# Kernel optimization log

Hardware: AMD Instinct MI355X
Metric: run time of the kernel (lower is better)

The kernel has to match this reference:

```python
import jax, jax.numpy as jnp
import numpy as np

E = 1024
H = 16
EPS = 1e-5


def setup_inputs() -> dict:
    key = jax.random.key(0)
    ks = jax.random.split(key, 17)
    B, T = 8, 1024
    s = 0.02
    inp = {
        'x': jax.random.normal(ks[0], (B, T, E), dtype=jnp.float32),
        'Wq': jax.random.normal(ks[1], (E, E), dtype=jnp.float32) * s,
        'bq': jnp.zeros((E,), jnp.float32),
        'Wk': jax.random.normal(ks[2], (E, E), dtype=jnp.float32) * s,
        'bk': jnp.zeros((E,), jnp.float32),
        'Wv': jax.random.normal(ks[3], (E, E), dtype=jnp.float32) * s,
        'bv': jnp.zeros((E,), jnp.float32),
        'Wo': jax.random.normal(ks[4], (E, E), dtype=jnp.float32) * s,
        'bo': jnp.zeros((E,), jnp.float32),
        'W1': jax.random.normal(ks[5], (E, 4 * E), dtype=jnp.float32) * s,
        'b1': jnp.zeros((4 * E,), jnp.float32),
        'W2': jax.random.normal(ks[6], (4 * E, E), dtype=jnp.float32) * s,
        'b2': jnp.zeros((E,), jnp.float32),
        'g1': jnp.ones((E,), jnp.float32),
        'be1': jnp.zeros((E,), jnp.float32),
        'g2': jnp.ones((E,), jnp.float32),
        'be2': jnp.zeros((E,), jnp.float32),
    }
    return inp


def _layernorm(x, g, b):
    mu = jnp.mean(x, axis=-1, keepdims=True)
    var = jnp.mean(jnp.square(x - mu), axis=-1, keepdims=True)
    return (x - mu) * jax.lax.rsqrt(var + EPS) * g + b


def _block(x, Wq, bq, Wk, bk, Wv, bv, Wo, bo, W1, b1, W2, b2, g1, be1, g2, be2):
    B, T, Ee = x.shape
    hd = Ee // H
    q = (x @ Wq + bq).reshape(B, T, H, hd).transpose(0, 2, 1, 3)  # (B,H,T,d)
    k = (x @ Wk + bk).reshape(B, T, H, hd).transpose(0, 2, 1, 3)
    v = (x @ Wv + bv).reshape(B, T, H, hd).transpose(0, 2, 1, 3)
    scores = jnp.einsum('bhqd,bhkd->bhqk', q, k) / jnp.sqrt(jnp.float32(hd))
    causal = jnp.tril(jnp.ones((T, T), bool))
    scores = jnp.where(causal, scores, -jnp.inf)
    w = jax.nn.softmax(scores, axis=-1)
    attn = jnp.einsum('bhqk,bhkd->bhqd', w, v)
    attn = attn.transpose(0, 2, 1, 3).reshape(B, T, Ee)
    attn = attn @ Wo + bo  # dropout is identity (p=0 / eval)
    x = _layernorm(x + attn, g1, be1)
    ff = jax.nn.relu(x @ W1 + b1) @ W2 + b2
    x = _layernorm(x + ff, g2, be2)
    return x


def reference(x, Wq, bq, Wk, bk, Wv, bv, Wo, bo, W1, b1, W2, b2, g1, be1, g2, be2):
    return _block(x, Wq, bq, Wk, bk, Wv, bv, Wo, bo, W1, b1, W2, b2, g1, be1, g2, be2)
```

## Files before the change

### kernel.cpp

```cpp
#include <hip/hip_runtime.h>
#include <math.h>

typedef unsigned short u16;
typedef __attribute__((ext_vector_type(8))) short short8;
typedef __attribute__((ext_vector_type(4))) float floatx4;

__device__ __forceinline__ u16 f2bf(float f) {
    unsigned u = __float_as_uint(f);
    unsigned r = u + 0x7fffu + ((u >> 16) & 1u);
    return (u16)(r >> 16);
}

__device__ __forceinline__ void gload16(const u16* g, u16* l) {
    __builtin_amdgcn_global_load_lds((const __attribute__((address_space(1))) void*)g,
                                     (__attribute__((address_space(3))) void*)l, 16, 0, 0);
}

template<int EPI>
__global__ __launch_bounds__(256) void gemm_mfma(
    const u16* __restrict__ A, const u16* __restrict__ Bt,
    const float* __restrict__ bias, const float* __restrict__ bias2,
    const float* __restrict__ bias3, const float* __restrict__ R,
    void* __restrict__ Cout, void* __restrict__ out2, void* __restrict__ out3,
    int M, int N, int K) {
    __shared__ u16 As[128 * 32];
    __shared__ u16 Bs[128 * 32];
    const int tid = threadIdx.x;
    const int wave = tid >> 6, lane = tid & 63;
    const int lrow = lane & 15, quad = lane >> 4;
    const int m0 = blockIdx.y * 128, n0 = blockIdx.x * 128;
    const int wm = (wave & 1) * 64, wn = (wave >> 1) * 64;

    floatx4 acc[4][4];
#pragma unroll
    for (int i = 0; i < 4; i++)
#pragma unroll
        for (int j = 0; j < 4; j++) acc[i][j] = {0.f, 0.f, 0.f, 0.f};

    const int f0 = wave * 128 + lane;

    for (int k0 = 0; k0 < K; k0 += 32) {
        __syncthreads();
#pragma unroll
        for (int i = 0; i < 2; i++) {
            int f = f0 + i * 64;
            int row = f >> 2, c = f & 3;
            int cg = c ^ ((row >> 1) & 3);
            gload16(A + (size_t)(m0 + row) * K + k0 + cg * 8, As + f * 8);
            gload16(Bt + (size_t)(n0 + row) * K + k0 + cg * 8, Bs + f * 8);
        }
        __syncthreads();
        short8 af[4], bf[4];
#pragma unroll
        for (int mt = 0; mt < 4; mt++) {
            int row = wm + mt * 16 + lrow;
            int ch = quad ^ ((lrow >> 1) & 3);
            af[mt] = *(const short8*)(As + row * 32 + ch * 8);
        }
#pragma unroll
        for (int nt = 0; nt < 4; nt++) {
            int row = wn + nt * 16 + lrow;
            int ch = quad ^ ((lrow >> 1) & 3);
            bf[nt] = *(const short8*)(Bs + row * 32 + ch * 8);
        }
#pragma unroll
        for (int mt = 0; mt < 4; mt++)
#pragma unroll
            for (int nt = 0; nt < 4; nt++)
                acc[mt][nt] = __builtin_amdgcn_mfma_f32_16x16x32_bf16(af[mt], bf[nt], acc[mt][nt], 0, 0, 0);
    }

    const float* bp = bias;
    int sec = 0;
    if (EPI == 4) {
        sec = n0 >> 10;
        bp = sec == 0 ? bias : (sec == 1 ? bias2 : bias3);
    }
    float bv[4];
#pragma unroll
    for (int nt = 0; nt < 4; nt++) {
        int gc = n0 + wn + nt * 16 + lrow;
        bv[nt] = bp[EPI == 4 ? (gc & 1023) : gc];
    }

#pragma unroll
    for (int mt = 0; mt < 4; mt++) {
        int gr0 = m0 + wm + mt * 16 + quad * 4;
#pragma unroll
        for (int nt = 0; nt < 4; nt++) {
            int gc = n0 + wn + nt * 16 + lrow;
            floatx4 a = acc[mt][nt];
            if (EPI == 1) {
                u16* C = (u16*)Cout;
#pragma unroll
                for (int r = 0; r < 4; r++)
                    C[(size_t)(gr0 + r) * N + gc] = f2bf(fmaxf(a[r] + bv[nt], 0.f));
            } else if (EPI == 2) {
                float* C = (float*)Cout;
#pragma unroll
                for (int r = 0; r < 4; r++) {
                    size_t idx = (size_t)(gr0 + r) * N + gc;
                    C[idx] = a[r] + bv[nt] + R[idx];
                }
            } else {
                int nc = gc & 1023;
                if (sec < 2) {
                    u16* C = (u16*)(sec == 0 ? Cout : out2);
#pragma unroll
                    for (int r = 0; r < 4; r++)
                        C[(size_t)(gr0 + r) * 1024 + nc] = f2bf(a[r] + bv[nt]);
                } else {
                    u16* C = (u16*)out3;
                    int bb = gr0 >> 10, t0 = gr0 & 1023;
                    size_t idx = ((size_t)(bb * 1024 + nc)) * 1024 + t0;
                    ushort4 u;
                    u.x = f2bf(a[0] + bv[nt]); u.y = f2bf(a[1] + bv[nt]);
                    u.z = f2bf(a[2] + bv[nt]); u.w = f2bf(a[3] + bv[nt]);
                    *(ushort4*)(C + idx) = u;
                }
            }
        }
    }
}

__global__ __launch_bounds__(256) void attn_mfma(
    const u16* __restrict__ q, const u16* __restrict__ k,
    const u16* __restrict__ vT, u16* __restrict__ o) {
    __shared__ u16 Kb[2][64 * 64];
    __shared__ u16 Vb[2][64 * 64];
    __shared__ u16 Pb[4][2][16 * 72];

    const int tid = threadIdx.x;
    const int wave = tid >> 6, lane = tid & 63;
    const int lrow = lane & 15, quad = lane >> 4;
    const int qb = blockIdx.x, bh = blockIdx.y;
    const int b = bh >> 4, h = bh & 15;
    const size_t tokbase = (size_t)b * 1024;
    const int ktmax = qb * 2 + 1;

#pragma unroll
    for (int i = 0; i < 2; i++) {
        int f = wave * 128 + i * 64 + lane;
        int row = f >> 3, c = f & 7, cg = c ^ (row & 7);
        gload16(q + (tokbase + qb * 128 + row) * 1024 + h * 64 + cg * 8, Kb[1] + f * 8);
        gload16(q + (tokbase + qb * 128 + 64 + row) * 1024 + h * 64 + cg * 8, Vb[1] + f * 8);
        gload16(k + (tokbase + row) * 1024 + h * 64 + cg * 8, Kb[0] + f * 8);
        gload16(vT + (tokbase + h * 64 + row) * 1024 + cg * 8, Vb[0] + f * 8);
    }
    asm volatile("s_waitcnt vmcnt(0)" ::: "memory");
    __syncthreads();
    short8 aQ[2][2];
#pragma unroll
    for (int band = 0; band < 2; band++)
#pragma unroll
        for (int ks = 0; ks < 2; ks++) {
            int row = wave * 16 + lrow;
            int pos = (ks * 4 + quad) ^ (lrow & 7);
            const u16* src = band ? Vb[1] : Kb[1];
            aQ[band][ks] = *(const short8*)(src + row * 64 + pos * 8);
        }
    __syncthreads();

    float lp[2][4];
    floatx4 oa[2][4];
#pragma unroll
    for (int bd = 0; bd < 2; bd++)
#pragma unroll
        for (int i = 0; i < 4; i++) { lp[bd][i] = 0.f; oa[bd][i] = {0.f, 0.f, 0.f, 0.f}; }

    for (int kt = 0; kt <= ktmax; kt++) {
        const int cur = kt & 1;
        if (kt < ktmax) {
            const int nxt = cur ^ 1;
#pragma unroll
            for (int i = 0; i < 2; i++) {
                int f = wave * 128 + i * 64 + lane;
                int row = f >> 3, c = f & 7, cg = c ^ (row & 7);
                gload16(k + (tokbase + (kt + 1) * 64 + row) * 1024 + h * 64 + cg * 8, Kb[nxt] + f * 8);
                gload16(vT + (tokbase + h * 64 + row) * 1024 + (kt + 1) * 64 + cg * 8, Vb[nxt] + f * 8);
            }
        }
#pragma unroll
        for (int band = 0; band < 2; band++) {
            const int btile = qb * 2 + band;
            if (kt > btile) continue;
            floatx4 sacc[4];
#pragma unroll
            for (int nt = 0; nt < 4; nt++) sacc[nt] = {0.f, 0.f, 0.f, 0.f};
#pragma unroll
            for (int nt = 0; nt < 4; nt++)
#pragma unroll
                for (int ks = 0; ks < 2; ks++) {
                    int row = nt * 16 + lrow;
                    int pos = (ks * 4 + quad) ^ (lrow & 7);
                    short8 bK = *(const short8*)(Kb[cur] + row * 64 + pos * 8);
                    sacc[nt] = __builtin_amdgcn_mfma_f32_16x16x32_bf16(aQ[band][ks], bK, sacc[nt], 0, 0, 0);
                }
            const bool diag = (kt == btile);
            float p[4][4];
#pragma unroll
            for (int r = 0; r < 4; r++) {
                int qrl = wave * 16 + quad * 4 + r;
#pragma unroll
                for (int nt = 0; nt < 4; nt++) {
                    float e = exp2f(sacc[nt][r] * 0.18033688011112042f);
                    if (diag && (nt * 16 + lrow) > qrl) e = 0.f;
                    p[nt][r] = e;
                    lp[band][r] += e;
                }
            }
            u16* Pw = Pb[wave][band];
#pragma unroll
            for (int nt = 0; nt < 4; nt++)
#pragma unroll
                for (int r = 0; r < 4; r++) {
                    int row = quad * 4 + r, key = nt * 16 + lrow;
                    int pos = ((key >> 3) ^ (row & 7)) * 8 + (key & 7);
                    Pw[row * 72 + pos] = f2bf(p[nt][r]);
                }
            asm volatile("s_waitcnt lgkmcnt(0)" ::: "memory");
            short8 aP[2];
#pragma unroll
            for (int ks = 0; ks < 2; ks++) {
                int pos = (ks * 4 + quad) ^ (lrow & 7);
                aP[ks] = *(const short8*)(Pw + lrow * 72 + pos * 8);
            }
#pragma unroll
            for (int nt = 0; nt < 4; nt++)
#pragma unroll
                for (int ks = 0; ks < 2; ks++) {
                    int row = nt * 16 + lrow;
                    int pos = (ks * 4 + quad) ^ (lrow & 7);
                    short8 bV = *(const short8*)(Vb[cur] + row * 64 + pos * 8);
                    oa[band][nt] = __builtin_amdgcn_mfma_f32_16x16x32_bf16(aP[ks], bV, oa[band][nt], 0, 0, 0);
                }
        }
        __syncthreads();
    }

#pragma unroll
    for (int band = 0; band < 2; band++) {
        float inv[4];
#pragma unroll
        for (int r = 0; r < 4; r++) {
            float l = lp[band][r];
#pragma unroll
            for (int off = 1; off < 16; off <<= 1) l += __shfl_xor(l, off);
            inv[r] = 1.f / l;
        }
#pragma unroll
        for (int nt = 0; nt < 4; nt++)
#pragma unroll
            for (int r = 0; r < 4; r++) {
                int grow = qb * 128 + band * 64 + wave * 16 + quad * 4 + r;
                float v = oa[band][nt][r] * inv[r];
                o[(tokbase + grow) * 1024 + h * 64 + nt * 16 + lrow] = f2bf(v);
            }
    }
}

__global__ __launch_bounds__(256) void f2bf_kernel(const float* __restrict__ in, u16* __restrict__ out) {
    size_t i = ((size_t)blockIdx.x * 256 + threadIdx.x) * 8;
    float4 a = *(const float4*)(in + i);
    float4 b = *(const float4*)(in + i + 4);
    ushort4 u0, u1;
    u0.x = f2bf(a.x); u0.y = f2bf(a.y); u0.z = f2bf(a.z); u0.w = f2bf(a.w);
    u1.x = f2bf(b.x); u1.y = f2bf(b.y); u1.z = f2bf(b.z); u1.w = f2bf(b.w);
    *(ushort4*)(out + i) = u0;
    *(ushort4*)(out + i + 4) = u1;
}

__global__ __launch_bounds__(256) void tconv_kernel(const float* __restrict__ W, u16* __restrict__ Wt,
                                                    int K, int N) {
    __shared__ float Ts[32][33];
    const int t = threadIdx.x;
    const int k0 = blockIdx.y * 32, n0 = blockIdx.x * 32;
    const int r = t >> 3, c4 = (t & 7) * 4;
    float4 v = *(const float4*)(W + (size_t)(k0 + r) * N + n0 + c4);
    Ts[c4 + 0][r] = v.x; Ts[c4 + 1][r] = v.y; Ts[c4 + 2][r] = v.z; Ts[c4 + 3][r] = v.w;
    __syncthreads();
    ushort4 u;
    u.x = f2bf(Ts[r][c4 + 0]); u.y = f2bf(Ts[r][c4 + 1]);
    u.z = f2bf(Ts[r][c4 + 2]); u.w = f2bf(Ts[r][c4 + 3]);
    *(ushort4*)(Wt + (size_t)(n0 + r) * K + k0 + c4) = u;
}

template<int WB>
__global__ __launch_bounds__(256) void ln_kernel(float* __restrict__ x, const float* __restrict__ g,
                                                 const float* __restrict__ bta, u16* __restrict__ xb) {
    __shared__ float red[8];
    const int tid = threadIdx.x;
    float* rowp = x + (size_t)blockIdx.x * 1024;
    float4 val = ((const float4*)rowp)[tid];

    float s = val.x + val.y + val.z + val.w;
#pragma unroll
    for (int off = 32; off; off >>= 1) s += __shfl_down(s, off);
    if ((tid & 63) == 0) red[tid >> 6] = s;
    __syncthreads();
    float mu = (red[0] + red[1] + red[2] + red[3]) * (1.f / 1024.f);

    float dx = val.x - mu, dy = val.y - mu, dz = val.z - mu, dw = val.w - mu;
    float sq = dx * dx + dy * dy + dz * dz + dw * dw;
#pragma unroll
    for (int off = 32; off; off >>= 1) sq += __shfl_down(sq, off);
    if ((tid & 63) == 0) red[4 + (tid >> 6)] = sq;
    __syncthreads();
    float var = (red[4] + red[5] + red[6] + red[7]) * (1.f / 1024.f);
    float rs = rsqrtf(var + 1e-5f);

    float4 gv = ((const float4*)g)[tid];
    float4 bv = ((const float4*)bta)[tid];
    float4 ov;
    ov.x = dx * rs * gv.x + bv.x;
    ov.y = dy * rs * gv.y + bv.y;
    ov.z = dz * rs * gv.z + bv.z;
    ov.w = dw * rs * gv.w + bv.w;
    ((float4*)rowp)[tid] = ov;
    if (WB) {
        u16* rb = xb + (size_t)blockIdx.x * 1024 + tid * 4;
        ushort4 u;
        u.x = f2bf(ov.x); u.y = f2bf(ov.y); u.z = f2bf(ov.z); u.w = f2bf(ov.w);
        *(ushort4*)rb = u;
    }
}

extern "C" void kernel_launch(void* const* d_in, const int* in_sizes, int n_in,
                              void* d_out, int out_size, void* d_ws, size_t ws_size,
                              hipStream_t stream) {
    const float* x   = (const float*)d_in[0];
    const float* Wq  = (const float*)d_in[1];
    const float* bq  = (const float*)d_in[2];
    const float* Wk  = (const float*)d_in[3];
    const float* bk  = (const float*)d_in[4];
    const float* Wv  = (const float*)d_in[5];
    const float* bv  = (const float*)d_in[6];
    const float* Wo  = (const float*)d_in[7];
    const float* bo  = (const float*)d_in[8];
    const float* W1  = (const float*)d_in[9];
    const float* b1  = (const float*)d_in[10];
    const float* W2  = (const float*)d_in[11];
    const float* b2  = (const float*)d_in[12];
    const float* g1  = (const float*)d_in[13];
    const float* be1 = (const float*)d_in[14];
    const float* g2  = (const float*)d_in[15];
    const float* be2 = (const float*)d_in[16];
    float* out = (float*)d_out;

    u16* w = (u16*)d_ws;
    const size_t SZ_ACT = (size_t)8192 * 1024;
    u16* xb    = w;                  w += SZ_ACT;
    u16* Wqkvt = w;                  w += (size_t)3 * 1024 * 1024;
    u16* Wot   = w;                  w += 1024 * 1024;
    u16* W1t   = w;                  w += (size_t)4096 * 1024;
    u16* W2t   = w;                  w += (size_t)1024 * 4096;
    u16* qb    = w;                  w += SZ_ACT;
    u16* kb    = w;                  w += SZ_ACT;
    u16* vTb   = w;                  w += SZ_ACT;
    u16* attb  = w;                  w += SZ_ACT;
    u16* hbuf  = qb;

    const int M = 8192;
    dim3 blk(256);

    f2bf_kernel<<<dim3(4096), blk, 0, stream>>>(x, xb);
    tconv_kernel<<<dim3(32, 32), blk, 0, stream>>>(Wq, Wqkvt, 1024, 1024);
    tconv_kernel<<<dim3(32, 32), blk, 0, stream>>>(Wk, Wqkvt + (size_t)1024 * 1024, 1024, 1024);
    tconv_kernel<<<dim3(32, 32), blk, 0, stream>>>(Wv, Wqkvt + (size_t)2048 * 1024, 1024, 1024);
    tconv_kernel<<<dim3(32, 32), blk, 0, stream>>>(Wo, Wot, 1024, 1024);
    tconv_kernel<<<dim3(128, 32), blk, 0, stream>>>(W1, W1t, 1024, 4096);
    tconv_kernel<<<dim3(32, 128), blk, 0, stream>>>(W2, W2t, 4096, 1024);

    gemm_mfma<4><<<dim3(24, 64), blk, 0, stream>>>(xb, Wqkvt, bq, bk, bv, nullptr,
                                                   qb, kb, vTb, M, 3072, 1024);
    attn_mfma<<<dim3(8, 128), blk, 0, stream>>>(qb, kb, vTb, attb);
    gemm_mfma<2><<<dim3(8, 64), blk, 0, stream>>>(attb, Wot, bo, nullptr, nullptr, x,
                                                  out, nullptr, nullptr, M, 1024, 1024);
    ln_kernel<1><<<dim3(8192), blk, 0, stream>>>(out, g1, be1, xb);
    gemm_mfma<1><<<dim3(32, 64), blk, 0, stream>>>(xb, W1t, b1, nullptr, nullptr, nullptr,
                                                   hbuf, nullptr, nullptr, M, 4096, 1024);
    gemm_mfma<2><<<dim3(8, 64), blk, 0, stream>>>(hbuf, W2t, b2, nullptr, nullptr, out,
                                                  out, nullptr, nullptr, M, 1024, 4096);
    ln_kernel<0><<<dim3(8192), blk, 0, stream>>>(out, g2, be2, nullptr);
}
```

Baseline: 572.5 us.

## Fuse prep conversions into one kernel and remap GEMM/attention block order

Result: faster. 522.8 us (-8.7%).

```diff
diff --git a/kernel.cpp b/kernel.cpp
--- a/kernel.cpp
+++ b/kernel.cpp
@@ -28,7 +28,9 @@
     const int tid = threadIdx.x;
     const int wave = tid >> 6, lane = tid & 63;
     const int lrow = lane & 15, quad = lane >> 4;
-    const int m0 = blockIdx.y * 128, n0 = blockIdx.x * 128;
+    const int ny = M >> 7;
+    const int by = blockIdx.x % ny, bx = blockIdx.x / ny;
+    const int m0 = by * 128, n0 = bx * 128;
     const int wm = (wave & 1) * 64, wn = (wave >> 1) * 64;
 
     floatx4 acc[4][4];
@@ -133,7 +135,7 @@
     const int tid = threadIdx.x;
     const int wave = tid >> 6, lane = tid & 63;
     const int lrow = lane & 15, quad = lane >> 4;
-    const int qb = blockIdx.x, bh = blockIdx.y;
+    const int qb = blockIdx.y, bh = blockIdx.x;
     const int b = bh >> 4, h = bh & 15;
     const size_t tokbase = (size_t)b * 1024;
     const int ktmax = qb * 2 + 1;
@@ -259,22 +261,9 @@
     }
 }
 
-__global__ __launch_bounds__(256) void f2bf_kernel(const float* __restrict__ in, u16* __restrict__ out) {
-    size_t i = ((size_t)blockIdx.x * 256 + threadIdx.x) * 8;
-    float4 a = *(const float4*)(in + i);
-    float4 b = *(const float4*)(in + i + 4);
-    ushort4 u0, u1;
-    u0.x = f2bf(a.x); u0.y = f2bf(a.y); u0.z = f2bf(a.z); u0.w = f2bf(a.w);
-    u1.x = f2bf(b.x); u1.y = f2bf(b.y); u1.z = f2bf(b.z); u1.w = f2bf(b.w);
-    *(ushort4*)(out + i) = u0;
-    *(ushort4*)(out + i + 4) = u1;
-}
-
-__global__ __launch_bounds__(256) void tconv_kernel(const float* __restrict__ W, u16* __restrict__ Wt,
-                                                    int K, int N) {
-    __shared__ float Ts[32][33];
-    const int t = threadIdx.x;
-    const int k0 = blockIdx.y * 32, n0 = blockIdx.x * 32;
+__device__ __forceinline__ void tconv_tile(const float* __restrict__ W, u16* __restrict__ Wt,
+                                           int K, int N, int k0, int n0, int t,
+                                           float (*Ts)[33]) {
     const int r = t >> 3, c4 = (t & 7) * 4;
     float4 v = *(const float4*)(W + (size_t)(k0 + r) * N + n0 + c4);
     Ts[c4 + 0][r] = v.x; Ts[c4 + 1][r] = v.y; Ts[c4 + 2][r] = v.z; Ts[c4 + 3][r] = v.w;
@@ -283,6 +272,40 @@
     u.x = f2bf(Ts[r][c4 + 0]); u.y = f2bf(Ts[r][c4 + 1]);
     u.z = f2bf(Ts[r][c4 + 2]); u.w = f2bf(Ts[r][c4 + 3]);
     *(ushort4*)(Wt + (size_t)(n0 + r) * K + k0 + c4) = u;
+}
+
+__global__ __launch_bounds__(256) void prep_kernel(
+    const float* __restrict__ x, const float* __restrict__ Wq, const float* __restrict__ Wk,
+    const float* __restrict__ Wv, const float* __restrict__ Wo, const float* __restrict__ W1,
+    const float* __restrict__ W2, u16* __restrict__ xb, u16* __restrict__ Wqkvt,
+    u16* __restrict__ Wot, u16* __restrict__ W1t, u16* __restrict__ W2t) {
+    __shared__ float Ts[32][33];
+    const int blk = blockIdx.x, t = threadIdx.x;
+    if (blk < 4096) {
+        size_t i = ((size_t)blk * 256 + t) * 8;
+        float4 a = *(const float4*)(x + i);
+        float4 b = *(const float4*)(x + i + 4);
+        ushort4 u0, u1;
+        u0.x = f2bf(a.x); u0.y = f2bf(a.y); u0.z = f2bf(a.z); u0.w = f2bf(a.w);
+        u1.x = f2bf(b.x); u1.y = f2bf(b.y); u1.z = f2bf(b.z); u1.w = f2bf(b.w);
+        *(ushort4*)(xb + i) = u0;
+        *(ushort4*)(xb + i + 4) = u1;
+    } else if (blk < 8192) {
+        int s = blk - 4096;
+        int which = s >> 10, tt = s & 1023;
+        int n0 = (tt & 31) * 32, k0 = (tt >> 5) * 32;
+        const float* W = which == 0 ? Wq : which == 1 ? Wk : which == 2 ? Wv : Wo;
+        u16* Wt = which == 3 ? Wot : Wqkvt + (size_t)which * 1024 * 1024;
+        tconv_tile(W, Wt, 1024, 1024, k0, n0, t, Ts);
+    } else if (blk < 12288) {
+        int tt = blk - 8192;
+        int n0 = (tt & 127) * 32, k0 = (tt >> 7) * 32;
+        tconv_tile(W1, W1t, 1024, 4096, k0, n0, t, Ts);
+    } else {
+        int tt = blk - 12288;
+        int n0 = (tt & 31) * 32, k0 = (tt >> 5) * 32;
+        tconv_tile(W2, W2t, 4096, 1024, k0, n0, t, Ts);
+    }
 }
 
 template<int WB>
@@ -363,23 +386,18 @@
     const int M = 8192;
     dim3 blk(256);
 
-    f2bf_kernel<<<dim3(4096), blk, 0, stream>>>(x, xb);
-    tconv_kernel<<<dim3(32, 32), blk, 0, stream>>>(Wq, Wqkvt, 1024, 1024);
-    tconv_kernel<<<dim3(32, 32), blk, 0, stream>>>(Wk, Wqkvt + (size_t)1024 * 1024, 1024, 1024);
-    tconv_kernel<<<dim3(32, 32), blk, 0, stream>>>(Wv, Wqkvt + (size_t)2048 * 1024, 1024, 1024);
-    tconv_kernel<<<dim3(32, 32), blk, 0, stream>>>(Wo, Wot, 1024, 1024);
-    tconv_kernel<<<dim3(128, 32), blk, 0, stream>>>(W1, W1t, 1024, 4096);
-    tconv_kernel<<<dim3(32, 128), blk, 0, stream>>>(W2, W2t, 4096, 1024);
-
-    gemm_mfma<4><<<dim3(24, 64), blk, 0, stream>>>(xb, Wqkvt, bq, bk, bv, nullptr,
-                                                   qb, kb, vTb, M, 3072, 1024);
-    attn_mfma<<<dim3(8, 128), blk, 0, stream>>>(qb, kb, vTb, attb);
-    gemm_mfma<2><<<dim3(8, 64), blk, 0, stream>>>(attb, Wot, bo, nullptr, nullptr, x,
-                                                  out, nullptr, nullptr, M, 1024, 1024);
+    prep_kernel<<<dim3(16384), blk, 0, stream>>>(x, Wq, Wk, Wv, Wo, W1, W2,
+                                                 xb, Wqkvt, Wot, W1t, W2t);
+
+    gemm_mfma<4><<<dim3(24 * 64), blk, 0, stream>>>(xb, Wqkvt, bq, bk, bv, nullptr,
+                                                    qb, kb, vTb, M, 3072, 1024);
+    attn_mfma<<<dim3(128, 8), blk, 0, stream>>>(qb, kb, vTb, attb);
+    gemm_mfma<2><<<dim3(8 * 64), blk, 0, stream>>>(attb, Wot, bo, nullptr, nullptr, x,
+                                                   out, nullptr, nullptr, M, 1024, 1024);
     ln_kernel<1><<<dim3(8192), blk, 0, stream>>>(out, g1, be1, xb);
-    gemm_mfma<1><<<dim3(32, 64), blk, 0, stream>>>(xb, W1t, b1, nullptr, nullptr, nullptr,
-                                                   hbuf, nullptr, nullptr, M, 4096, 1024);
-    gemm_mfma<2><<<dim3(8, 64), blk, 0, stream>>>(hbuf, W2t, b2, nullptr, nullptr, out,
-                                                  out, nullptr, nullptr, M, 1024, 4096);
+    gemm_mfma<1><<<dim3(32 * 64), blk, 0, stream>>>(xb, W1t, b1, nullptr, nullptr, nullptr,
+                                                    hbuf, nullptr, nullptr, M, 4096, 1024);
+    gemm_mfma<2><<<dim3(8 * 64), blk, 0, stream>>>(hbuf, W2t, b2, nullptr, nullptr, out,
+                                                   out, nullptr, nullptr, M, 1024, 4096);
     ln_kernel<0><<<dim3(8192), blk, 0, stream>>>(out, g2, be2, nullptr);
 }
```
